# Kernel tuning notes

Hardware: AMD Instinct MI355X
Metric: run time of the kernel (lower is better)

Reference implementation:

```python
import jax, jax.numpy as jnp
import numpy as np

N_BUCKETS = 16
EMBD = 1024
VOCAB = 32000
SEQ_LEN = 2048
RANK = 8
BUCKET_SIZE = max(1, SEQ_LEN // N_BUCKETS)


def setup_inputs() -> dict:
    key = jax.random.key(0)
    k1, k2, k3 = jax.random.split(key, 3)
    hidden = jax.random.normal(k1, (2, SEQ_LEN, EMBD), dtype=jnp.float32)
    A = jax.random.normal(k2, (N_BUCKETS, EMBD, RANK), dtype=jnp.float32) * 0.01
    B = jax.random.normal(k3, (RANK, VOCAB), dtype=jnp.float32) * 0.01
    alpha = jnp.asarray(0.05, dtype=jnp.float32)
    return {"hidden": hidden, "A": A, "B": B, "alpha": alpha}


def reference(hidden, A, B, alpha):
    # bucket index per time step: t // bucket_size, clamped to n_buckets-1
    T = hidden.shape[1]
    bucket_idx = jnp.minimum(jnp.arange(T) // BUCKET_SIZE, N_BUCKETS - 1)
    # gather per-position low-rank A: [T, E, R]
    A_t = A[bucket_idx]
    # per-token low-rank projection: [B, T, R]
    low = jnp.einsum('bte,ter->btr', hidden, A_t)
    # project to vocab and scale: [B, T, V]
    return alpha * jnp.einsum('btr,rv->btv', low, B)
```

## Files before the change

kernel.cpp:

```cpp
#include <hip/hip_runtime.h>

#define SEQ_LEN 2048
#define EMBD 1024
#define VOCAB 32000
#define RANK 8
#define N_ROWS (2 * SEQ_LEN)
#define T_TILE 64
#define V4_PER_ROW (VOCAB / 4)

typedef float v4f __attribute__((ext_vector_type(4)));

__global__ __launch_bounds__(256) void low_kernel(const float* __restrict__ hidden,
                                                  const float* __restrict__ A,
                                                  const float* __restrict__ alpha_p,
                                                  float* __restrict__ low) {
    const int row = blockIdx.x;
    const int t = row & (SEQ_LEN - 1);
    const int bucket = t >> 7;
    const int tid = threadIdx.x;
    const float alpha = alpha_p[0];

    const float* h  = hidden + (size_t)row * EMBD;
    const float* Ab = A + (size_t)bucket * EMBD * RANK;

    float acc[RANK];
#pragma unroll
    for (int r = 0; r < RANK; ++r) acc[r] = 0.f;

    const int e0 = tid * 4;
    const float4 hv = *reinterpret_cast<const float4*>(h + e0);
#pragma unroll
    for (int j = 0; j < 4; ++j) {
        const float hval = (&hv.x)[j];
        const float* Ar = Ab + (size_t)(e0 + j) * RANK;
        const float4 a0 = *reinterpret_cast<const float4*>(Ar);
        const float4 a1 = *reinterpret_cast<const float4*>(Ar + 4);
        acc[0] += hval * a0.x; acc[1] += hval * a0.y;
        acc[2] += hval * a0.z; acc[3] += hval * a0.w;
        acc[4] += hval * a1.x; acc[5] += hval * a1.y;
        acc[6] += hval * a1.z; acc[7] += hval * a1.w;
    }

#pragma unroll
    for (int r = 0; r < RANK; ++r) {
#pragma unroll
        for (int off = 32; off > 0; off >>= 1)
            acc[r] += __shfl_down(acc[r], off, 64);
    }

    __shared__ float partial[4][RANK];
    const int wave = tid >> 6;
    const int lane = tid & 63;
    if (lane == 0) {
#pragma unroll
        for (int r = 0; r < RANK; ++r) partial[wave][r] = acc[r];
    }
    __syncthreads();
    if (tid < RANK) {
        const float s = partial[0][tid] + partial[1][tid] + partial[2][tid] + partial[3][tid];
        low[(size_t)row * RANK + tid] = alpha * s;
    }
}

__global__ __launch_bounds__(256) void proj_kernel(const float* __restrict__ low,
                                                   const float* __restrict__ B,
                                                   float* __restrict__ out) {
    const int v4 = blockIdx.x * 256 + threadIdx.x;
    const int row0 = blockIdx.y * T_TILE;

    __shared__ float slow[T_TILE * RANK];
    for (int i = threadIdx.x; i < T_TILE * RANK; i += 256)
        slow[i] = low[(size_t)row0 * RANK + i];
    __syncthreads();

    if (v4 >= V4_PER_ROW) return;
    const int v = v4 * 4;

    float4 b[RANK];
#pragma unroll
    for (int r = 0; r < RANK; ++r)
        b[r] = *reinterpret_cast<const float4*>(B + (size_t)r * VOCAB + v);

    const float4* slow4 = reinterpret_cast<const float4*>(slow);
    float* outp = out + (size_t)row0 * VOCAB + v;

#pragma unroll 8
    for (int tt = 0; tt < T_TILE; ++tt) {
        const float4 l0 = slow4[tt * 2];
        const float4 l1 = slow4[tt * 2 + 1];
        v4f o;
        o.x = l0.x * b[0].x + l0.y * b[1].x + l0.z * b[2].x + l0.w * b[3].x
            + l1.x * b[4].x + l1.y * b[5].x + l1.z * b[6].x + l1.w * b[7].x;
        o.y = l0.x * b[0].y + l0.y * b[1].y + l0.z * b[2].y + l0.w * b[3].y
            + l1.x * b[4].y + l1.y * b[5].y + l1.z * b[6].y + l1.w * b[7].y;
        o.z = l0.x * b[0].z + l0.y * b[1].z + l0.z * b[2].z + l0.w * b[3].z
            + l1.x * b[4].z + l1.y * b[5].z + l1.z * b[6].z + l1.w * b[7].z;
        o.w = l0.x * b[0].w + l0.y * b[1].w + l0.z * b[2].w + l0.w * b[3].w
            + l1.x * b[4].w + l1.y * b[5].w + l1.z * b[6].w + l1.w * b[7].w;
        __builtin_nontemporal_store(o, reinterpret_cast<v4f*>(outp));
        outp += VOCAB;
    }
}

extern "C" void kernel_launch(void* const* d_in, const int* in_sizes, int n_in,
                              void* d_out, int out_size, void* d_ws, size_t ws_size,
                              hipStream_t stream) {
    const float* hidden = (const float*)d_in[0];
    const float* A      = (const float*)d_in[1];
    const float* B      = (const float*)d_in[2];
    const float* alpha  = (const float*)d_in[3];
    float* out = (float*)d_out;
    float* low = (float*)d_ws;

    low_kernel<<<N_ROWS, 256, 0, stream>>>(hidden, A, alpha, low);

    dim3 grid((V4_PER_ROW + 255) / 256, N_ROWS / T_TILE);
    proj_kernel<<<grid, 256, 0, stream>>>(low, B, out);
}
```

Baseline: 536.7 us.

## Fuse low-rank projection into vocab projection kernel, recomputing per block

Merges the two kernels into one: each block computes the rank-8 projection for its 64 rows into shared memory, then writes its vocab slice. This removes the intermediate workspace round trip and one launch. In exchange, every vocab-column block recomputes the same low rows, re-reading the hidden rows and A for each of the 32 column blocks. It also adds occupancy hints and lowers the unroll factor.

```diff
diff --git a/kernel.cpp b/kernel.cpp
--- a/kernel.cpp
+++ b/kernel.cpp
@@ -10,69 +10,64 @@
 
 typedef float v4f __attribute__((ext_vector_type(4)));
 
-__global__ __launch_bounds__(256) void low_kernel(const float* __restrict__ hidden,
-                                                  const float* __restrict__ A,
-                                                  const float* __restrict__ alpha_p,
-                                                  float* __restrict__ low) {
-    const int row = blockIdx.x;
-    const int t = row & (SEQ_LEN - 1);
-    const int bucket = t >> 7;
-    const int tid = threadIdx.x;
+__global__ __launch_bounds__(256, 4) void fused_kernel(
+    const float* __restrict__ hidden,
+    const float* __restrict__ A,
+    const float* __restrict__ B,
+    const float* __restrict__ alpha_p,
+    float* __restrict__ out)
+{
+    const int row0 = blockIdx.y * T_TILE;
+    const int t0 = row0 & (SEQ_LEN - 1);
+    const int bucket = t0 >> 7;
+    const int tid  = threadIdx.x;
+    const int wave = tid >> 6;
+    const int lane = tid & 63;
+
+    __shared__ float slow[T_TILE][RANK];
+
     const float alpha = alpha_p[0];
+    const float* __restrict__ Ab = A + (size_t)bucket * (EMBD * RANK);
+    const float* __restrict__ hbase = hidden + (size_t)(row0 + wave * 16) * EMBD;
 
-    const float* h  = hidden + (size_t)row * EMBD;
-    const float* Ab = A + (size_t)bucket * EMBD * RANK;
-
-    float acc[RANK];
+    for (int rr = 0; rr < 16; ++rr) {
+        const float* h = hbase + (size_t)rr * EMBD;
+        float acc[RANK];
 #pragma unroll
-    for (int r = 0; r < RANK; ++r) acc[r] = 0.f;
-
-    const int e0 = tid * 4;
-    const float4 hv = *reinterpret_cast<const float4*>(h + e0);
-#pragma unroll
-    for (int j = 0; j < 4; ++j) {
-        const float hval = (&hv.x)[j];
-        const float* Ar = Ab + (size_t)(e0 + j) * RANK;
-        const float4 a0 = *reinterpret_cast<const float4*>(Ar);
-        const float4 a1 = *reinterpret_cast<const float4*>(Ar + 4);
-        acc[0] += hval * a0.x; acc[1] += hval * a0.y;
-        acc[2] += hval * a0.z; acc[3] += hval * a0.w;
-        acc[4] += hval * a1.x; acc[5] += hval * a1.y;
-        acc[6] += hval * a1.z; acc[7] += hval * a1.w;
-    }
+        for (int r = 0; r < RANK; ++r) acc[r] = 0.f;
 
 #pragma unroll
-    for (int r = 0; r < RANK; ++r) {
+        for (int q = 0; q < 4; ++q) {
+            const int e = q * 256 + lane * 4;
+            const float4 hv = *reinterpret_cast<const float4*>(h + e);
 #pragma unroll
-        for (int off = 32; off > 0; off >>= 1)
-            acc[r] += __shfl_down(acc[r], off, 64);
-    }
+            for (int j = 0; j < 4; ++j) {
+                const float hval = (&hv.x)[j];
+                const float* Ar = Ab + (size_t)(e + j) * RANK;
+                const float4 a0 = *reinterpret_cast<const float4*>(Ar);
+                const float4 a1 = *reinterpret_cast<const float4*>(Ar + 4);
+                acc[0] += hval * a0.x; acc[1] += hval * a0.y;
+                acc[2] += hval * a0.z; acc[3] += hval * a0.w;
+                acc[4] += hval * a1.x; acc[5] += hval * a1.y;
+                acc[6] += hval * a1.z; acc[7] += hval * a1.w;
+            }
+        }
 
-    __shared__ float partial[4][RANK];
-    const int wave = tid >> 6;
-    const int lane = tid & 63;
-    if (lane == 0) {
 #pragma unroll
-        for (int r = 0; r < RANK; ++r) partial[wave][r] = acc[r];
+        for (int r = 0; r < RANK; ++r) {
+#pragma unroll
+            for (int off = 32; off > 0; off >>= 1)
+                acc[r] += __shfl_down(acc[r], off, 64);
+        }
+        if (lane == 0) {
+#pragma unroll
+            for (int r = 0; r < RANK; ++r)
+                slow[wave * 16 + rr][r] = alpha * acc[r];
+        }
     }
     __syncthreads();
-    if (tid < RANK) {
-        const float s = partial[0][tid] + partial[1][tid] + partial[2][tid] + partial[3][tid];
-        low[(size_t)row * RANK + tid] = alpha * s;
-    }
-}
 
-__global__ __launch_bounds__(256) void proj_kernel(const float* __restrict__ low,
-                                                   const float* __restrict__ B,
-                                                   float* __restrict__ out) {
-    const int v4 = blockIdx.x * 256 + threadIdx.x;
-    const int row0 = blockIdx.y * T_TILE;
-
-    __shared__ float slow[T_TILE * RANK];
-    for (int i = threadIdx.x; i < T_TILE * RANK; i += 256)
-        slow[i] = low[(size_t)row0 * RANK + i];
-    __syncthreads();
-
+    const int v4 = blockIdx.x * 256 + tid;
     if (v4 >= V4_PER_ROW) return;
     const int v = v4 * 4;
 
@@ -81,13 +76,12 @@
     for (int r = 0; r < RANK; ++r)
         b[r] = *reinterpret_cast<const float4*>(B + (size_t)r * VOCAB + v);
 
-    const float4* slow4 = reinterpret_cast<const float4*>(slow);
     float* outp = out + (size_t)row0 * VOCAB + v;
 
-#pragma unroll 8
+#pragma unroll 2
     for (int tt = 0; tt < T_TILE; ++tt) {
-        const float4 l0 = slow4[tt * 2];
-        const float4 l1 = slow4[tt * 2 + 1];
+        const float4 l0 = *reinterpret_cast<const float4*>(&slow[tt][0]);
+        const float4 l1 = *reinterpret_cast<const float4*>(&slow[tt][4]);
         v4f o;
         o.x = l0.x * b[0].x + l0.y * b[1].x + l0.z * b[2].x + l0.w * b[3].x
             + l1.x * b[4].x + l1.y * b[5].x + l1.z * b[6].x + l1.w * b[7].x;
@@ -110,10 +104,7 @@
     const float* B      = (const float*)d_in[2];
     const float* alpha  = (const float*)d_in[3];
     float* out = (float*)d_out;
-    float* low = (float*)d_ws;
-
-    low_kernel<<<N_ROWS, 256, 0, stream>>>(hidden, A, alpha, low);
 
     dim3 grid((V4_PER_ROW + 255) / 256, N_ROWS / T_TILE);
-    proj_kernel<<<grid, 256, 0, stream>>>(low, B, out);
+    fused_kernel<<<grid, 256, 0, stream>>>(hidden, A, B, alpha, out);
 }
```

After: 697.3 us. 29.9% more time.
